# Performance work log

Measured on AMD Instinct MI355X. Metric: run time of the kernel, lower is better.

Reference implementation:

```python
import jax, jax.numpy as jnp
import numpy as np

N = 100000   # nodes
E = 625000   # edges
D = 128      # feature dim (layers = [128,128,128])
H = 8        # attention heads
HD = 16      # head dim (H*HD == D)


def setup_inputs() -> dict:
    key = jax.random.key(0)
    ks = jax.random.split(key, 16)
    s = 1.0 / np.sqrt(D).astype(np.float32)
    inp = {
        'x': jax.random.normal(ks[0], (N, D), dtype=jnp.float32),
        'edge_index': jax.random.randint(ks[1], (2, E), 0, N, dtype=jnp.int64),
        'W1': jax.random.normal(ks[2], (D, D), dtype=jnp.float32) * s,
        'b1': jnp.zeros((D,), jnp.float32),
        'W2': jax.random.normal(ks[3], (D, D), dtype=jnp.float32) * s,
        'b2': jnp.zeros((D,), jnp.float32),
        'Wq': jax.random.normal(ks[4], (D, H * HD), dtype=jnp.float32) * s,
        'bq': jnp.zeros((H * HD,), jnp.float32),
        'Wk': jax.random.normal(ks[5], (D, H * HD), dtype=jnp.float32) * s,
        'bk': jnp.zeros((H * HD,), jnp.float32),
        'Wv': jax.random.normal(ks[6], (D, H * HD), dtype=jnp.float32) * s,
        'bv': jnp.zeros((H * HD,), jnp.float32),
        'Wo': jax.random.normal(ks[7], (H * HD, D), dtype=jnp.float32) * s,
        'bo': jnp.zeros((D,), jnp.float32),
    }
    return inp


def _gcn_conv(x, W, b, src, dst):
    """PyG GCNConv: x' = D^-1/2 (A+I) D^-1/2 (x W) + b, symmetric norm with self-loops."""
    h = x @ W                                   # [N, Dout]
    # degree at targets, +1 for self-loop
    deg = jnp.ones((N,), h.dtype).at[dst].add(jnp.ones((E,), h.dtype))
    dinv = jax.lax.rsqrt(deg)                   # [N]
    norm = dinv[src] * dinv[dst]                # [E]
    agg = jnp.zeros_like(h).at[dst].add(h[src] * norm[:, None])
    agg = agg + h * (dinv * dinv)[:, None]      # self-loop term
    return agg + b


def _mha_seq1(x, Wq, bq, Wk, bk, Wv, bv, Wo, bo):
    """Faithful to the hand-rolled MHA: batch=N, implied seq_len=1."""
    n = x.shape[0]
    q = (x @ Wq + bq).reshape(n, 1, H, HD).transpose(0, 2, 1, 3)  # [N,H,1,HD]
    k = (x @ Wk + bk).reshape(n, 1, H, HD).transpose(0, 2, 1, 3)
    v = (x @ Wv + bv).reshape(n, 1, H, HD).transpose(0, 2, 1, 3)
    scores = jnp.einsum('nhqd,nhkd->nhqk', q, k) / np.float32(np.sqrt(HD))
    attn = jax.nn.softmax(scores, axis=-1)                        # [N,H,1,1]
    out = jnp.einsum('nhqk,nhkd->nhqd', attn, v)                  # [N,H,1,HD]
    out = out.transpose(0, 2, 1, 3).reshape(n, 1, H * HD)
    return out @ Wo + bo                                          # [N,1,D]


def reference(x, edge_index, W1, b1, W2, b2, Wq, bq, Wk, bk, Wv, bv, Wo, bo):
    src, dst = edge_index[0], edge_index[1]
    h = _gcn_conv(x, W1, b1, src, dst)
    h = jax.nn.relu(h)                 # dropout is identity in eval
    h = _gcn_conv(h, W2, b2, src, dst) # last conv: no relu
    return _mha_seq1(h, Wq, bq, Wk, bk, Wv, bv, Wo, bo)
```

## Files before the change

kernel.cpp:

```cpp
#include <hip/hip_runtime.h>
#include <hip/hip_bf16.h>

#define DD 128

typedef __bf16 bf16x8v __attribute__((ext_vector_type(8)));
typedef float  f32x4   __attribute__((ext_vector_type(4)));

__device__ inline unsigned short f2bf(float f) {
    unsigned u = __builtin_bit_cast(unsigned, f);
    unsigned r = (u + 0x7fffu + ((u >> 16) & 1u)) >> 16;
    return (unsigned short)r;
}
__device__ inline float bflo2f(unsigned p) { return __builtin_bit_cast(float, p << 16); }
__device__ inline float bfhi2f(unsigned p) { return __builtin_bit_cast(float, p & 0xffff0000u); }
__device__ inline float rl_f(int v, int i) {
    return __builtin_bit_cast(float, __builtin_amdgcn_readlane(v, i));
}

__global__ __launch_bounds__(256) void k_zero(int* __restrict__ a, int* __restrict__ b, int N) {
    int i = blockIdx.x * 256 + threadIdx.x;
    int stride = gridDim.x * 256;
    for (; i < N; i += stride) { a[i] = 0; b[i] = 0; }
}

__global__ __launch_bounds__(256) void k_hist_fuse1(const int* __restrict__ dst, int* __restrict__ cnt,
                                                    int E, int N,
                                                    const float* __restrict__ Wv, const float* __restrict__ Wo,
                                                    const float* __restrict__ bv, const float* __restrict__ bo,
                                                    float* __restrict__ Wf, float* __restrict__ bfo, int EB) {
    if ((int)blockIdx.x < EB) {
        int e = blockIdx.x * 256 + threadIdx.x;
        if (e < E) {
            int d = dst[e];
            if ((unsigned)d < (unsigned)N) atomicAdd(&cnt[d], 1);
        }
    } else {
        int gid = (blockIdx.x - EB) * 256 + threadIdx.x;
        if (gid >= (DD + 1) * DD) return;
        int i = gid >> 7, j = gid & (DD - 1);
        if (i < DD) {
            float acc = 0.f;
            for (int k = 0; k < DD; ++k) acc = fmaf(Wv[i * DD + k], Wo[k * DD + j], acc);
            Wf[i * DD + j] = acc;
        } else {
            float acc = bo[j];
            for (int k = 0; k < DD; ++k) acc = fmaf(bv[k], Wo[k * DD + j], acc);
            bfo[j] = acc;
        }
    }
}

__global__ __launch_bounds__(256) void k_scanblk_wprep(const int* __restrict__ cnt, int* __restrict__ rowptr,
                                                       int* __restrict__ bsums, int N, int nb,
                                                       const float* __restrict__ W2, const float* __restrict__ Wf,
                                                       const float* __restrict__ b2, const float* __restrict__ bfo,
                                                       unsigned short* __restrict__ W2ft, float* __restrict__ bf2,
                                                       const float* __restrict__ W1, unsigned short* __restrict__ Wt1) {
    if ((int)blockIdx.x < nb) {
        __shared__ int sh[256];
        int t = threadIdx.x;
        int gid = blockIdx.x * 256 + t;
        int v = (gid < N) ? cnt[gid] : 0;
        sh[t] = v;
        __syncthreads();
        #pragma unroll
        for (int off = 1; off < 256; off <<= 1) {
            int add = (t >= off) ? sh[t - off] : 0;
            __syncthreads();
            sh[t] += add;
            __syncthreads();
        }
        if (gid < N) rowptr[gid] = sh[t] - v;
        if (t == 255) bsums[blockIdx.x] = sh[255];
    } else {
        int blk = blockIdx.x - nb;
        if (blk < 65) {
            int gid = blk * 256 + threadIdx.x;
            if (gid >= (DD + 1) * DD) return;
            int i = gid >> 7, j = gid & (DD - 1);
            if (i < DD) {
                float acc = 0.f;
                for (int k = 0; k < DD; ++k) acc = fmaf(W2[i * DD + k], Wf[k * DD + j], acc);
                W2ft[j * DD + i] = f2bf(acc);
            } else {
                float acc = bfo[j];
                for (int k = 0; k < DD; ++k) acc = fmaf(b2[k], Wf[k * DD + j], acc);
                bf2[j] = acc;
            }
        } else {
            int gid = (blk - 65) * 256 + threadIdx.x;
            int k = gid >> 7, n = gid & 127;
            Wt1[n * DD + k] = f2bf(W1[k * DD + n]);
        }
    }
}

__global__ __launch_bounds__(256) void k_scan_add2(int* __restrict__ rowptr, const int* __restrict__ bsums,
                                                   const int* __restrict__ cnt, float* __restrict__ dinv,
                                                   int N, int nb) {
    __shared__ int sh[512];
    int t = threadIdx.x;
    sh[t]       = (t < nb)       ? bsums[t]       : 0;
    sh[t + 256] = (t + 256 < nb) ? bsums[t + 256] : 0;
    __syncthreads();
    #pragma unroll
    for (int off = 1; off < 512; off <<= 1) {
        int a = (t >= off)       ? sh[t - off]       : 0;
        int b = (t + 256 >= off) ? sh[t + 256 - off] : 0;
        __syncthreads();
        sh[t] += a;
        sh[t + 256] += b;
        __syncthreads();
    }
    int b = blockIdx.x;
    int pfx = (b == 0) ? 0 : sh[b - 1];
    int gid = b * 256 + t;
    if (gid < N) {
        int c = cnt[gid];
        int v = rowptr[gid] + pfx;
        rowptr[gid] = v;
        if (gid == N - 1) rowptr[N] = v + c;
        dinv[gid] = rsqrtf(1.0f + (float)c);
    }
}

__global__ __launch_bounds__(256) void k_fill(const int* __restrict__ src, const int* __restrict__ dst,
                                              const int* __restrict__ rowptr, int* __restrict__ fillc,
                                              const float* __restrict__ dinv,
                                              int2* __restrict__ ev, int E, int N) {
    int e = blockIdx.x * 256 + threadIdx.x;
    if (e >= E) return;
    int s = src[e], d = dst[e];
    if ((unsigned)s >= (unsigned)N || (unsigned)d >= (unsigned)N) return;
    int pos = rowptr[d] + atomicAdd(&fillc[d], 1);
    float nm = dinv[s] * dinv[d];
    ev[pos] = make_int2(s, __builtin_bit_cast(int, nm));
}

template<int AF32>
__global__ __launch_bounds__(256, 2) void k_gemm_mfma(const void* __restrict__ Av,
                                                      const unsigned short* __restrict__ Wt,
                                                      unsigned short* __restrict__ Cb, int M) {
    int w  = threadIdx.x >> 6;
    int l  = threadIdx.x & 63;
    int lr = l & 15, lg = l >> 4;

    bf16x8v bfr[8][4];
    #pragma unroll
    for (int nt = 0; nt < 8; ++nt)
        #pragma unroll
        for (int kk = 0; kk < 4; ++kk)
            bfr[nt][kk] = *reinterpret_cast<const bf16x8v*>(Wt + (nt * 16 + lr) * DD + kk * 32 + lg * 8);

    int tiles = (M + 63) >> 6;
    for (int t = blockIdx.x; t < tiles; t += gridDim.x) {
        int m0 = t * 64 + w * 16;
        int row = m0 + lr;
        int rowc = row < M ? row : (M - 1);

        bf16x8v af[4];
        if (AF32) {
            const float* Af = (const float*)Av;
            #pragma unroll
            for (int kk = 0; kk < 4; ++kk) {
                const float* p = Af + (size_t)rowc * DD + kk * 32 + lg * 8;
                float4 u0 = *reinterpret_cast<const float4*>(p);
                float4 u1 = *reinterpret_cast<const float4*>(p + 4);
                af[kk][0] = (__bf16)u0.x; af[kk][1] = (__bf16)u0.y;
                af[kk][2] = (__bf16)u0.z; af[kk][3] = (__bf16)u0.w;
                af[kk][4] = (__bf16)u1.x; af[kk][5] = (__bf16)u1.y;
                af[kk][6] = (__bf16)u1.z; af[kk][7] = (__bf16)u1.w;
            }
        } else {
            const unsigned short* Ab = (const unsigned short*)Av;
            #pragma unroll
            for (int kk = 0; kk < 4; ++kk)
                af[kk] = *reinterpret_cast<const bf16x8v*>(Ab + (size_t)rowc * DD + kk * 32 + lg * 8);
        }

        f32x4 acc[8] = {};
        #pragma unroll
        for (int kk = 0; kk < 4; ++kk)
            #pragma unroll
            for (int nt = 0; nt < 8; ++nt)
                acc[nt] = __builtin_amdgcn_mfma_f32_16x16x32_bf16(af[kk], bfr[nt][kk], acc[nt], 0, 0, 0);

        #pragma unroll
        for (int nt = 0; nt < 8; ++nt)
            #pragma unroll
            for (int r = 0; r < 4; ++r) {
                int rr = m0 + lg * 4 + r;
                if (rr < M) Cb[(size_t)rr * DD + nt * 16 + lr] = f2bf(acc[nt][r]);
            }
    }
}

template<int OUTF32, int RELU>
__global__ __launch_bounds__(256) void k_gather8(const int* __restrict__ rowptr, const int2* __restrict__ ev,
                                                 const unsigned* __restrict__ h32, const float* __restrict__ dinv,
                                                 const float* __restrict__ bias, void* __restrict__ outp, int N) {
    int l = threadIdx.x & 63;
    int g = blockIdx.x * 4 + (threadIdx.x >> 6);
    int m0 = g * 8;
    if (m0 >= N) return;
    float2 bb = reinterpret_cast<const float2*>(bias)[l];

    int rpidx = m0 + l; if (rpidx > N) rpidx = N;
    int rp = (l < 9) ? rowptr[rpidx] : 0;
    int dvidx = m0 + l; if (dvidx >= N) dvidx = N - 1;
    float dv = (l < 8) ? dinv[dvidx] : 0.f;

    int2 me0, me1;
    {
        int b0 = __builtin_amdgcn_readlane(rp, 0), e0 = __builtin_amdgcn_readlane(rp, 1);
        int c0 = e0 - b0; if (c0 > 64) c0 = 64;
        me0 = (c0 > 0) ? ev[b0 + (l < c0 ? l : c0 - 1)] : make_int2(0, 0);
        int b1 = e0, e1 = __builtin_amdgcn_readlane(rp, 2);
        int c1 = e1 - b1; if (c1 > 64) c1 = 64;
        me1 = (c1 > 0) ? ev[b1 + (l < c1 ? l : c1 - 1)] : make_int2(0, 0);
    }

    #pragma unroll
    for (int r = 0; r < 8; r += 2) {
        int nA = m0 + r, nB = m0 + r + 1;
        int bA = __builtin_amdgcn_readlane(rp, r);
        int eA = __builtin_amdgcn_readlane(rp, r + 1);
        int eB = __builtin_amdgcn_readlane(rp, r + 2);
        int degA = eA - bA, degB = eB - eA;
        int bB = eA;
        int2 mA = me0, mB = me1;
        if (r + 2 < 8) {
            int b2 = __builtin_amdgcn_readlane(rp, r + 2), e2 = __builtin_amdgcn_readlane(rp, r + 3);
            int c2 = e2 - b2; if (c2 > 64) c2 = 64;
            me0 = (c2 > 0) ? ev[b2 + (l < c2 ? l : c2 - 1)] : make_int2(0, 0);
            int b3 = e2, e3 = __builtin_amdgcn_readlane(rp, r + 4);
            int c3 = e3 - b3; if (c3 > 64) c3 = 64;
            me1 = (c3 > 0) ? ev[b3 + (l < c3 ? l : c3 - 1)] : make_int2(0, 0);
        }

        int cA = degA < 64 ? degA : 64;
        int cB = degB < 64 ? degB : 64;
        int fA = cA < 8 ? cA : 8;
        int fB = cB < 8 ? cB : 8;

        unsigned pA[8], pB[8]; float wA[8], wB[8];
        #pragma unroll
        for (int q = 0; q < 8; ++q) {
            int ia = (q < fA) ? q : (fA > 0 ? fA - 1 : 0);
            int s = __builtin_amdgcn_readlane(mA.x, ia);
            pA[q] = h32[(size_t)s * 64 + l];
            wA[q] = (q < fA) ? rl_f(mA.y, ia) : 0.f;
        }
        #pragma unroll
        for (int q = 0; q < 8; ++q) {
            int ib = (q < fB) ? q : (fB > 0 ? fB - 1 : 0);
            int s = __builtin_amdgcn_readlane(mB.x, ib);
            pB[q] = h32[(size_t)s * 64 + l];
            wB[q] = (q < fB) ? rl_f(mB.y, ib) : 0.f;
        }
        unsigned psA = h32[(size_t)(nA < N ? nA : N - 1) * 64 + l];
        unsigned psB = h32[(size_t)(nB < N ? nB : N - 1) * 64 + l];

        float axA = 0.f, ayA = 0.f, axB = 0.f, ayB = 0.f;
        #pragma unroll
        for (int q = 0; q < 8; ++q) {
            axA = fmaf(wA[q], bflo2f(pA[q]), axA);
            ayA = fmaf(wA[q], bfhi2f(pA[q]), ayA);
            axB = fmaf(wB[q], bflo2f(pB[q]), axB);
            ayB = fmaf(wB[q], bfhi2f(pB[q]), ayB);
        }

        for (int i = 8; i < cA; i += 8) {
            #pragma unroll
            for (int q = 0; q < 8; ++q) {
                int ia = (i + q < cA) ? i + q : cA - 1;
                int s = __builtin_amdgcn_readlane(mA.x, ia);
                unsigned p = h32[(size_t)s * 64 + l];
                float wq = (i + q < cA) ? rl_f(mA.y, ia) : 0.f;
                axA = fmaf(wq, bflo2f(p), axA);
                ayA = fmaf(wq, bfhi2f(p), ayA);
            }
        }
        for (int i = 8; i < cB; i += 8) {
            #pragma unroll
            for (int q = 0; q < 8; ++q) {
                int ib = (i + q < cB) ? i + q : cB - 1;
                int s = __builtin_amdgcn_readlane(mB.x, ib);
                unsigned p = h32[(size_t)s * 64 + l];
                float wq = (i + q < cB) ? rl_f(mB.y, ib) : 0.f;
                axB = fmaf(wq, bflo2f(p), axB);
                ayB = fmaf(wq, bfhi2f(p), ayB);
            }
        }
        for (int base = 64; base < degA; base += 64) {
            int cc = degA - base; if (cc > 64) cc = 64;
            int2 m2 = ev[bA + base + (l < cc ? l : cc - 1)];
            for (int ii = 0; ii < cc; ++ii) {
                int s = __builtin_amdgcn_readlane(m2.x, ii);
                unsigned p = h32[(size_t)s * 64 + l];
                float wq = rl_f(m2.y, ii);
                axA = fmaf(wq, bflo2f(p), axA);
                ayA = fmaf(wq, bfhi2f(p), ayA);
            }
        }
        for (int base = 64; base < degB; base += 64) {
            int cc = degB - base; if (cc > 64) cc = 64;
            int2 m2 = ev[bB + base + (l < cc ? l : cc - 1)];
            for (int ii = 0; ii < cc; ++ii) {
                int s = __builtin_amdgcn_readlane(m2.x, ii);
                unsigned p = h32[(size_t)s * 64 + l];
                float wq = rl_f(m2.y, ii);
                axB = fmaf(wq, bflo2f(p), axB);
                ayB = fmaf(wq, bfhi2f(p), ayB);
            }
        }

        if (nA < N) {
            float di = __builtin_bit_cast(float, __builtin_amdgcn_readlane(__builtin_bit_cast(int, dv), r));
            float di2 = di * di;
            float ox = fmaf(di2, bflo2f(psA), axA) + bb.x;
            float oy = fmaf(di2, bfhi2f(psA), ayA) + bb.y;
            if (RELU) { ox = fmaxf(ox, 0.f); oy = fmaxf(oy, 0.f); }
            if (OUTF32) reinterpret_cast<float2*>(outp)[(size_t)nA * 64 + l] = make_float2(ox, oy);
            else {
                unsigned po = (unsigned)f2bf(ox) | ((unsigned)f2bf(oy) << 16);
                reinterpret_cast<unsigned*>(outp)[(size_t)nA * 64 + l] = po;
            }
        }
        if (nB < N) {
            float di = __builtin_bit_cast(float, __builtin_amdgcn_readlane(__builtin_bit_cast(int, dv), r + 1));
            float di2 = di * di;
            float ox = fmaf(di2, bflo2f(psB), axB) + bb.x;
            float oy = fmaf(di2, bfhi2f(psB), ayB) + bb.y;
            if (RELU) { ox = fmaxf(ox, 0.f); oy = fmaxf(oy, 0.f); }
            if (OUTF32) reinterpret_cast<float2*>(outp)[(size_t)nB * 64 + l] = make_float2(ox, oy);
            else {
                unsigned po = (unsigned)f2bf(ox) | ((unsigned)f2bf(oy) << 16);
                reinterpret_cast<unsigned*>(outp)[(size_t)nB * 64 + l] = po;
            }
        }
    }
}

extern "C" void kernel_launch(void* const* d_in, const int* in_sizes, int n_in,
                              void* d_out, int out_size, void* d_ws, size_t ws_size,
                              hipStream_t stream) {
    const float* x  = (const float*)d_in[0];
    const int*   ei = (const int*)d_in[1];
    const float* W1 = (const float*)d_in[2];
    const float* b1 = (const float*)d_in[3];
    const float* W2 = (const float*)d_in[4];
    const float* b2 = (const float*)d_in[5];
    const float* Wv = (const float*)d_in[10];
    const float* bv = (const float*)d_in[11];
    const float* Wo = (const float*)d_in[12];
    const float* bo = (const float*)d_in[13];
    int N = in_sizes[0] / DD;
    int E = in_sizes[1] / 2;
    const int* src = ei;
    const int* dst = ei + E;
    float* out = (float*)d_out;

    unsigned* hA  = (unsigned*)d_ws;
    unsigned* h1  = hA + (size_t)N * 64;
    float* dinv   = (float*)(h1 + (size_t)N * 64);
    float* Wf     = dinv + N;
    float* bfo    = Wf + DD * DD;
    float* bf2    = bfo + DD;
    unsigned short* Wt1  = (unsigned short*)(bf2 + DD);
    unsigned short* W2ft = Wt1 + DD * DD;
    int* cnt    = (int*)(W2ft + DD * DD);
    int* fillc  = cnt + N;
    int* rowptr = fillc + N;
    int* bsums  = rowptr + N + 1;
    int2* ev    = (int2*)(((uintptr_t)(bsums + 512) + 15) & ~(uintptr_t)15);

    int nb = (N + 255) / 256;
    int EB = (E + 255) / 256;

    k_zero<<<512, 256, 0, stream>>>(cnt, fillc, N);
    k_hist_fuse1<<<EB + 129, 256, 0, stream>>>(dst, cnt, E, N, Wv, Wo, bv, bo, Wf, bfo, EB);
    k_scanblk_wprep<<<nb + 129, 256, 0, stream>>>(cnt, rowptr, bsums, N, nb,
                                                  W2, Wf, b2, bfo, W2ft, bf2, W1, Wt1);
    k_scan_add2<<<nb, 256, 0, stream>>>(rowptr, bsums, cnt, dinv, N, nb);
    k_fill<<<EB, 256, 0, stream>>>(src, dst, rowptr, fillc, dinv, ev, E, N);
    k_gemm_mfma<1><<<512, 256, 0, stream>>>(x, Wt1, (unsigned short*)hA, N);
    int gb = ((N + 7) / 8 + 3) / 4;
    k_gather8<0, 1><<<gb, 256, 0, stream>>>(rowptr, ev, hA, dinv, b1, h1, N);
    k_gemm_mfma<0><<<512, 256, 0, stream>>>(h1, W2ft, (unsigned short*)hA, N);
    k_gather8<1, 0><<<gb, 256, 0, stream>>>(rowptr, ev, hA, dinv, bf2, out, N);
}
```

Measured before the change: 188.9 us.

## Gather four nodes per wave with all first-8 neighbor loads issued together

Replaces the 8-nodes-per-wave gather, which handled two nodes per iteration with a software-prefetched edge list, with a 4-nodes-per-wave kernel. The new kernel loads all four edge lists up front and issues the first 8 neighbor row loads for all four nodes (32 gathers) before any accumulation. The aim is more memory-level parallelism per wave and twice as many waves to spread over the GPU. In exchange it needs more registers per thread, which may lower occupancy, and it drops the cross-pair prefetch.

```diff
diff --git a/kernel.cpp b/kernel.cpp
--- a/kernel.cpp
+++ b/kernel.cpp
@@ -196,147 +196,102 @@
 }
 
 template<int OUTF32, int RELU>
-__global__ __launch_bounds__(256) void k_gather8(const int* __restrict__ rowptr, const int2* __restrict__ ev,
+__global__ __launch_bounds__(256) void k_gather4(const int* __restrict__ rowptr, const int2* __restrict__ ev,
                                                  const unsigned* __restrict__ h32, const float* __restrict__ dinv,
                                                  const float* __restrict__ bias, void* __restrict__ outp, int N) {
     int l = threadIdx.x & 63;
     int g = blockIdx.x * 4 + (threadIdx.x >> 6);
-    int m0 = g * 8;
+    int m0 = g * 4;
     if (m0 >= N) return;
     float2 bb = reinterpret_cast<const float2*>(bias)[l];
 
     int rpidx = m0 + l; if (rpidx > N) rpidx = N;
-    int rp = (l < 9) ? rowptr[rpidx] : 0;
+    int rp = (l < 5) ? rowptr[rpidx] : 0;
     int dvidx = m0 + l; if (dvidx >= N) dvidx = N - 1;
-    float dv = (l < 8) ? dinv[dvidx] : 0.f;
-
-    int2 me0, me1;
-    {
-        int b0 = __builtin_amdgcn_readlane(rp, 0), e0 = __builtin_amdgcn_readlane(rp, 1);
-        int c0 = e0 - b0; if (c0 > 64) c0 = 64;
-        me0 = (c0 > 0) ? ev[b0 + (l < c0 ? l : c0 - 1)] : make_int2(0, 0);
-        int b1 = e0, e1 = __builtin_amdgcn_readlane(rp, 2);
-        int c1 = e1 - b1; if (c1 > 64) c1 = 64;
-        me1 = (c1 > 0) ? ev[b1 + (l < c1 ? l : c1 - 1)] : make_int2(0, 0);
-    }
-
-    #pragma unroll
-    for (int r = 0; r < 8; r += 2) {
-        int nA = m0 + r, nB = m0 + r + 1;
-        int bA = __builtin_amdgcn_readlane(rp, r);
-        int eA = __builtin_amdgcn_readlane(rp, r + 1);
-        int eB = __builtin_amdgcn_readlane(rp, r + 2);
-        int degA = eA - bA, degB = eB - eA;
-        int bB = eA;
-        int2 mA = me0, mB = me1;
-        if (r + 2 < 8) {
-            int b2 = __builtin_amdgcn_readlane(rp, r + 2), e2 = __builtin_amdgcn_readlane(rp, r + 3);
-            int c2 = e2 - b2; if (c2 > 64) c2 = 64;
-            me0 = (c2 > 0) ? ev[b2 + (l < c2 ? l : c2 - 1)] : make_int2(0, 0);
-            int b3 = e2, e3 = __builtin_amdgcn_readlane(rp, r + 4);
-            int c3 = e3 - b3; if (c3 > 64) c3 = 64;
-            me1 = (c3 > 0) ? ev[b3 + (l < c3 ? l : c3 - 1)] : make_int2(0, 0);
-        }
-
-        int cA = degA < 64 ? degA : 64;
-        int cB = degB < 64 ? degB : 64;
-        int fA = cA < 8 ? cA : 8;
-        int fB = cB < 8 ? cB : 8;
-
-        unsigned pA[8], pB[8]; float wA[8], wB[8];
+    float dv = (l < 4) ? dinv[dvidx] : 0.f;
+
+    int bs[5];
+    #pragma unroll
+    for (int i = 0; i < 5; ++i) bs[i] = __builtin_amdgcn_readlane(rp, i);
+
+    int deg[4], c[4];
+    int2 me[4];
+    #pragma unroll
+    for (int r = 0; r < 4; ++r) {
+        deg[r] = bs[r + 1] - bs[r];
+        int cc = deg[r] > 64 ? 64 : deg[r];
+        c[r] = cc;
+        me[r] = (cc > 0) ? ev[bs[r] + (l < cc ? l : cc - 1)] : make_int2(0, 0);
+    }
+
+    unsigned p[4][8]; float w[4][8];
+    #pragma unroll
+    for (int r = 0; r < 4; ++r) {
+        int f = c[r] < 8 ? c[r] : 8;
         #pragma unroll
         for (int q = 0; q < 8; ++q) {
-            int ia = (q < fA) ? q : (fA > 0 ? fA - 1 : 0);
-            int s = __builtin_amdgcn_readlane(mA.x, ia);
-            pA[q] = h32[(size_t)s * 64 + l];
-            wA[q] = (q < fA) ? rl_f(mA.y, ia) : 0.f;
-        }
+            int i = (q < f) ? q : (f > 0 ? f - 1 : 0);
+            int s = __builtin_amdgcn_readlane(me[r].x, i);
+            p[r][q] = h32[(size_t)s * 64 + l];
+            w[r][q] = (q < f) ? rl_f(me[r].y, i) : 0.f;
+        }
+    }
+    unsigned ps[4];
+    #pragma unroll
+    for (int r = 0; r < 4; ++r) {
+        int n = m0 + r; int nc = n < N ? n : N - 1;
+        ps[r] = h32[(size_t)nc * 64 + l];
+    }
+
+    float ax[4] = {0.f, 0.f, 0.f, 0.f}, ay[4] = {0.f, 0.f, 0.f, 0.f};
+    #pragma unroll
+    for (int r = 0; r < 4; ++r)
         #pragma unroll
         for (int q = 0; q < 8; ++q) {
-            int ib = (q < fB) ? q : (fB > 0 ? fB - 1 : 0);
-            int s = __builtin_amdgcn_readlane(mB.x, ib);
-            pB[q] = h32[(size_t)s * 64 + l];
-            wB[q] = (q < fB) ? rl_f(mB.y, ib) : 0.f;
-        }
-        unsigned psA = h32[(size_t)(nA < N ? nA : N - 1) * 64 + l];
-        unsigned psB = h32[(size_t)(nB < N ? nB : N - 1) * 64 + l];
-
-        float axA = 0.f, ayA = 0.f, axB = 0.f, ayB = 0.f;
-        #pragma unroll
-        for (int q = 0; q < 8; ++q) {
-            axA = fmaf(wA[q], bflo2f(pA[q]), axA);
-            ayA = fmaf(wA[q], bfhi2f(pA[q]), ayA);
-            axB = fmaf(wB[q], bflo2f(pB[q]), axB);
-            ayB = fmaf(wB[q], bfhi2f(pB[q]), ayB);
-        }
-
-        for (int i = 8; i < cA; i += 8) {
+            ax[r] = fmaf(w[r][q], bflo2f(p[r][q]), ax[r]);
+            ay[r] = fmaf(w[r][q], bfhi2f(p[r][q]), ay[r]);
+        }
+
+    #pragma unroll
+    for (int r = 0; r < 4; ++r) {
+        for (int i = 8; i < c[r]; i += 8) {
             #pragma unroll
             for (int q = 0; q < 8; ++q) {
-                int ia = (i + q < cA) ? i + q : cA - 1;
-                int s = __builtin_amdgcn_readlane(mA.x, ia);
-                unsigned p = h32[(size_t)s * 64 + l];
-                float wq = (i + q < cA) ? rl_f(mA.y, ia) : 0.f;
-                axA = fmaf(wq, bflo2f(p), axA);
-                ayA = fmaf(wq, bfhi2f(p), ayA);
-            }
-        }
-        for (int i = 8; i < cB; i += 8) {
-            #pragma unroll
-            for (int q = 0; q < 8; ++q) {
-                int ib = (i + q < cB) ? i + q : cB - 1;
-                int s = __builtin_amdgcn_readlane(mB.x, ib);
-                unsigned p = h32[(size_t)s * 64 + l];
-                float wq = (i + q < cB) ? rl_f(mB.y, ib) : 0.f;
-                axB = fmaf(wq, bflo2f(p), axB);
-                ayB = fmaf(wq, bfhi2f(p), ayB);
-            }
-        }
-        for (int base = 64; base < degA; base += 64) {
-            int cc = degA - base; if (cc > 64) cc = 64;
-            int2 m2 = ev[bA + base + (l < cc ? l : cc - 1)];
+                int ii = (i + q < c[r]) ? i + q : c[r] - 1;
+                int s = __builtin_amdgcn_readlane(me[r].x, ii);
+                unsigned pp = h32[(size_t)s * 64 + l];
+                float wq = (i + q < c[r]) ? rl_f(me[r].y, ii) : 0.f;
+                ax[r] = fmaf(wq, bflo2f(pp), ax[r]);
+                ay[r] = fmaf(wq, bfhi2f(pp), ay[r]);
+            }
+        }
+        for (int base = 64; base < deg[r]; base += 64) {
+            int cc = deg[r] - base; if (cc > 64) cc = 64;
+            int2 m2 = ev[bs[r] + base + (l < cc ? l : cc - 1)];
             for (int ii = 0; ii < cc; ++ii) {
                 int s = __builtin_amdgcn_readlane(m2.x, ii);
-                unsigned p = h32[(size_t)s * 64 + l];
+                unsigned pp = h32[(size_t)s * 64 + l];
                 float wq = rl_f(m2.y, ii);
-                axA = fmaf(wq, bflo2f(p), axA);
-                ayA = fmaf(wq, bfhi2f(p), ayA);
-            }
-        }
-        for (int base = 64; base < degB; base += 64) {
-            int cc = degB - base; if (cc > 64) cc = 64;
-            int2 m2 = ev[bB + base + (l < cc ? l : cc - 1)];
-            for (int ii = 0; ii < cc; ++ii) {
-                int s = __builtin_amdgcn_readlane(m2.x, ii);
-                unsigned p = h32[(size_t)s * 64 + l];
-                float wq = rl_f(m2.y, ii);
-                axB = fmaf(wq, bflo2f(p), axB);
-                ayB = fmaf(wq, bfhi2f(p), ayB);
-            }
-        }
-
-        if (nA < N) {
+                ax[r] = fmaf(wq, bflo2f(pp), ax[r]);
+                ay[r] = fmaf(wq, bfhi2f(pp), ay[r]);
+            }
+        }
+    }
+
+    #pragma unroll
+    for (int r = 0; r < 4; ++r) {
+        int n = m0 + r;
+        if (n < N) {
             float di = __builtin_bit_cast(float, __builtin_amdgcn_readlane(__builtin_bit_cast(int, dv), r));
             float di2 = di * di;
-            float ox = fmaf(di2, bflo2f(psA), axA) + bb.x;
-            float oy = fmaf(di2, bfhi2f(psA), ayA) + bb.y;
+            float ox = fmaf(di2, bflo2f(ps[r]), ax[r]) + bb.x;
+            float oy = fmaf(di2, bfhi2f(ps[r]), ay[r]) + bb.y;
             if (RELU) { ox = fmaxf(ox, 0.f); oy = fmaxf(oy, 0.f); }
-            if (OUTF32) reinterpret_cast<float2*>(outp)[(size_t)nA * 64 + l] = make_float2(ox, oy);
-            else {
+            if (OUTF32) {
+                reinterpret_cast<float2*>(outp)[(size_t)n * 64 + l] = make_float2(ox, oy);
+            } else {
                 unsigned po = (unsigned)f2bf(ox) | ((unsigned)f2bf(oy) << 16);
-                reinterpret_cast<unsigned*>(outp)[(size_t)nA * 64 + l] = po;
-            }
-        }
-        if (nB < N) {
-            float di = __builtin_bit_cast(float, __builtin_amdgcn_readlane(__builtin_bit_cast(int, dv), r + 1));
-            float di2 = di * di;
-            float ox = fmaf(di2, bflo2f(psB), axB) + bb.x;
-            float oy = fmaf(di2, bfhi2f(psB), ayB) + bb.y;
-            if (RELU) { ox = fmaxf(ox, 0.f); oy = fmaxf(oy, 0.f); }
-            if (OUTF32) reinterpret_cast<float2*>(outp)[(size_t)nB * 64 + l] = make_float2(ox, oy);
-            else {
-                unsigned po = (unsigned)f2bf(ox) | ((unsigned)f2bf(oy) << 16);
-                reinterpret_cast<unsigned*>(outp)[(size_t)nB * 64 + l] = po;
+                reinterpret_cast<unsigned*>(outp)[(size_t)n * 64 + l] = po;
             }
         }
     }
@@ -385,8 +340,8 @@
     k_scan_add2<<<nb, 256, 0, stream>>>(rowptr, bsums, cnt, dinv, N, nb);
     k_fill<<<EB, 256, 0, stream>>>(src, dst, rowptr, fillc, dinv, ev, E, N);
     k_gemm_mfma<1><<<512, 256, 0, stream>>>(x, Wt1, (unsigned short*)hA, N);
-    int gb = ((N + 7) / 8 + 3) / 4;
-    k_gather8<0, 1><<<gb, 256, 0, stream>>>(rowptr, ev, hA, dinv, b1, h1, N);
+    int gb = (N + 15) / 16;
+    k_gather4<0, 1><<<gb, 256, 0, stream>>>(rowptr, ev, hA, dinv, b1, h1, N);
     k_gemm_mfma<0><<<512, 256, 0, stream>>>(h1, W2ft, (unsigned short*)hA, N);
-    k_gather8<1, 0><<<gb, 256, 0, stream>>>(rowptr, ev, hA, dinv, bf2, out, N);
-}
+    k_gather4<1, 0><<<gb, 256, 0, stream>>>(rowptr, ev, hA, dinv, bf2, out, N);
+}
```

New measurement: 186.9 us. About the same (-1.0%).
